# Kernel tuning notes

Measured on AMD Instinct MI355X. Metric: run time of the kernel, lower is better.

The kernel has to match this reference:

```python
import jax, jax.numpy as jnp
import numpy as np

B, N0 = 16384, 2048
NUM_CLASSES, NUM_CLUSTERS, NDIM = 12, 24, 4
W_SCALE = 0.02  # keep logits in a sane range for softmax


def setup_inputs() -> dict:
    key = jax.random.key(0)
    ks = jax.random.split(key, 7)
    return {
        "x": jax.random.normal(ks[0], (B, N0), dtype=jnp.float32),
        "W_fc": jax.random.normal(ks[1], (N0, NUM_CLASSES), dtype=jnp.float32) * W_SCALE,
        "b_fc": jax.random.normal(ks[2], (NUM_CLASSES,), dtype=jnp.float32) * W_SCALE,
        "W_bin": jax.random.normal(ks[3], (NUM_CLASSES, N0, NUM_CLUSTERS), dtype=jnp.float32) * W_SCALE,
        "b_bin": jax.random.normal(ks[4], (NUM_CLASSES, NUM_CLUSTERS), dtype=jnp.float32) * W_SCALE,
        "W_res": jax.random.normal(ks[5], (NUM_CLASSES, N0, NDIM), dtype=jnp.float32) * W_SCALE,
        "b_res": jax.random.normal(ks[6], (NUM_CLASSES, NDIM), dtype=jnp.float32) * W_SCALE,
    }


def reference(x, W_fc, b_fc, W_bin, b_bin, W_res, b_res):
    # x: [B, N0] pre-extracted features (feature_model output)
    bsz = x.shape[0]
    C = W_bin.shape[0]

    # category head
    y0 = x @ W_fc + b_fc                                   # [B, C]
    Pc = jax.nn.softmax(y0, axis=1)                        # [B, C]

    # grouped per-class bin linears as one batched GEMM -> [B, K, C]
    y1 = jnp.einsum('bd,cdk->bkc', x, W_bin) + b_bin.T[None]
    Pl = jax.nn.softmax(y1, axis=1)                        # softmax over clusters
    Plc = Pl * Pc[:, None, :]                              # [B, K, C]

    # joint argmax over (cluster, class); torch flatten of [B,K,C] -> ic = ind % C
    ind = jnp.argmax(Plc.reshape(bsz, -1), axis=1)
    ic = ind % C                                           # selected class per row

    # direct gather replaces one-hot scatter + bmm
    y1_sel = jnp.take_along_axis(y1, ic[:, None, None], axis=2)[..., 0]   # [B, K]

    # grouped per-class residual linears -> [B, ndim, C], then gather
    y2 = jnp.einsum('bd,cdn->bnc', x, W_res) + b_res.T[None]
    y2_sel = jnp.take_along_axis(y2, ic[:, None, None], axis=2)[..., 0]   # [B, ndim]

    return (y0, y1_sel, y2_sel, Plc)
```

## Files before the change

### kernel.cpp

```cpp
#include <hip/hip_runtime.h>
#include <math.h>

#define BROWS 16384
#define N0    2048
#define NCLS  12
#define NCLU  24
#define NDIM  4
#define NCOL  348
#define NPAD  384
#define NTILE 24

#define OUT0_OFF 0
#define OUT1_OFF (BROWS * NCLS)
#define OUT2_OFF (OUT1_OFF + BROWS * NCLU)
#define OUT3_OFF (OUT2_OFF + BROWS * NDIM)

typedef __attribute__((ext_vector_type(8))) short bf16x8;
typedef __attribute__((ext_vector_type(4))) float f32x4;
typedef unsigned short ushort_t;

__device__ __forceinline__ unsigned short f2bf(float f) {
    unsigned u = __float_as_uint(f);
    u += 0x7fffu + ((u >> 16) & 1u);
    return (unsigned short)(u >> 16);
}
__device__ __forceinline__ float bf2f(unsigned short h) {
    return __uint_as_float(((unsigned)h) << 16);
}
__device__ __forceinline__ void cvt8(float4 a, float4 b, bf16x8& h, bf16x8& l) {
    float f[8] = {a.x, a.y, a.z, a.w, b.x, b.y, b.z, b.w};
    #pragma unroll
    for (int i = 0; i < 8; ++i) {
        unsigned short hi = f2bf(f[i]);
        h[i] = (short)hi;
        l[i] = (short)f2bf(f[i] - bf2f(hi));
    }
}

__device__ __forceinline__ void load_lds16(const void* g, void* l) {
    __builtin_amdgcn_global_load_lds((const __attribute__((address_space(1))) void*)g,
                                     (__attribute__((address_space(3))) void*)l, 16, 0, 0);
}

__device__ __forceinline__ float fused_w(const float* __restrict__ W_fc,
                                         const float* __restrict__ W_bin,
                                         const float* __restrict__ W_res,
                                         int col, int d) {
    float w = 0.0f;
    if (col < NCLS) {
        w = W_fc[d * NCLS + col];
    } else if (col < 12 + NCLU * NCLS) {
        int jj = col - 12;
        int k = jj / NCLS, c = jj - k * NCLS;
        w = W_bin[((size_t)c * N0 + d) * NCLU + k];
    } else if (col < NCOL) {
        int jj = col - 300;
        int n = jj / NCLS, c = jj - n * NCLS;
        w = W_res[((size_t)c * N0 + d) * NDIM + n];
    }
    return w;
}

__global__ void jcp_repack3(const float* __restrict__ W_fc, const float* __restrict__ b_fc,
                            const float* __restrict__ W_bin, const float* __restrict__ b_bin,
                            const float* __restrict__ W_res, const float* __restrict__ b_res,
                            ushort_t* __restrict__ Bph, ushort_t* __restrict__ Bpl,
                            float* __restrict__ bias) {
    int t = blockIdx.x * 256 + threadIdx.x;
    if (t >= NTILE * 64 * 64) return;
    const int lane = t & 63;
    const int kb   = (t >> 6) & 63;
    const int J    = t >> 12;
    const int col  = J * 16 + (lane & 15);
    const int k0   = kb * 32 + (lane >> 4) * 8;

    bf16x8 h, l;
    #pragma unroll
    for (int i = 0; i < 8; ++i) {
        float w = fused_w(W_fc, W_bin, W_res, col, k0 + i);
        unsigned short hi = f2bf(w);
        h[i] = (short)hi;
        l[i] = (short)f2bf(w - bf2f(hi));
    }
    *(bf16x8*)(Bph + (size_t)t * 8) = h;
    *(bf16x8*)(Bpl + (size_t)t * 8) = l;

    if (t < NPAD) {
        int jb = t;
        float bv = 0.0f;
        if (jb < NCLS) {
            bv = b_fc[jb];
        } else if (jb < 12 + NCLU * NCLS) {
            int jj = jb - 12;
            int k = jj / NCLS, c = jj - k * NCLS;
            bv = b_bin[c * NCLU + k];
        } else if (jb < NCOL) {
            int jj = jb - 300;
            int n = jj / NCLS, c = jj - n * NCLS;
            bv = b_res[c * NDIM + n];
        }
        bias[jb] = bv;
    }
}

__global__ __launch_bounds__(256, 4) void jcp_gemm4(const float* __restrict__ x,
                                                    const ushort_t* __restrict__ Bph,
                                                    const ushort_t* __restrict__ Bpl,
                                                    const float* __restrict__ bias,
                                                    float* __restrict__ Y) {
    __shared__ float Lx[2 * 2048];

    const int tid  = threadIdx.x;
    const int wid  = tid >> 6;
    const int lane = tid & 63;
    const int quad = lane >> 4;
    const int l16  = lane & 15;
    const int wrow = (wid & 1) * 32;
    const int wct  = (wid >> 1) * 3;
    const int rbase = blockIdx.y * 64;
    const int jbase = blockIdx.x * 96;

    const int dr = lane >> 3;
    const int dc = (lane & 7) ^ dr;
    const float* gsrc0 = x + (size_t)(rbase + 8 * (2 * wid) + dr) * N0 + dc * 4;
    const float* gsrc1 = x + (size_t)(rbase + 8 * (2 * wid + 1) + dr) * N0 + dc * 4;
    const int ldst0 = (2 * wid) * 256;
    const int ldst1 = (2 * wid + 1) * 256;

    const int s = l16 & 7;
    const int pos1 = (2 * quad) ^ s;
    const int o1 = pos1 * 4;
    const int o2 = (pos1 ^ 1) * 4;
    const int ro0 = (wrow + l16) * 32;
    const int ro1 = (wrow + 16 + l16) * 32;

    const ushort_t* pBh = Bph + (size_t)lane * 8;
    const ushort_t* pBl = Bpl + (size_t)lane * 8;
    int Jt[3];
    #pragma unroll
    for (int j = 0; j < 3; ++j) Jt[j] = (jbase / 16 + wct + j) * 32768;

    f32x4 acc[2][3];
    #pragma unroll
    for (int i = 0; i < 2; ++i)
        #pragma unroll
        for (int j = 0; j < 3; ++j)
            acc[i][j] = f32x4{0.f, 0.f, 0.f, 0.f};

    load_lds16(gsrc0, &Lx[ldst0]);
    load_lds16(gsrc1, &Lx[ldst1]);
    __syncthreads();

    int p = 0;
    for (int it = 0; it < 64; ++it) {
        bf16x8 bh[3], bl[3];
        #pragma unroll
        for (int j = 0; j < 3; ++j) {
            bh[j] = *(const bf16x8*)(pBh + Jt[j] + it * 512);
            bl[j] = *(const bf16x8*)(pBl + Jt[j] + it * 512);
        }
        if (it < 63) {
            load_lds16(gsrc0 + (it + 1) * 32, &Lx[(p ^ 1) * 2048 + ldst0]);
            load_lds16(gsrc1 + (it + 1) * 32, &Lx[(p ^ 1) * 2048 + ldst1]);
        }
        const int pb = p * 2048;
        float4 f0a = *(const float4*)&Lx[pb + ro0 + o1];
        float4 f0b = *(const float4*)&Lx[pb + ro0 + o2];
        float4 f1a = *(const float4*)&Lx[pb + ro1 + o1];
        float4 f1b = *(const float4*)&Lx[pb + ro1 + o2];
        bf16x8 Ah[2], Al[2];
        cvt8(f0a, f0b, Ah[0], Al[0]);
        cvt8(f1a, f1b, Ah[1], Al[1]);

        #pragma unroll
        for (int j = 0; j < 3; ++j)
            #pragma unroll
            for (int i = 0; i < 2; ++i) {
                acc[i][j] = __builtin_amdgcn_mfma_f32_16x16x32_bf16(Ah[i], bh[j], acc[i][j], 0, 0, 0);
                acc[i][j] = __builtin_amdgcn_mfma_f32_16x16x32_bf16(Al[i], bh[j], acc[i][j], 0, 0, 0);
                acc[i][j] = __builtin_amdgcn_mfma_f32_16x16x32_bf16(Ah[i], bl[j], acc[i][j], 0, 0, 0);
            }
        __syncthreads();
        p ^= 1;
    }

    #pragma unroll
    for (int j = 0; j < 3; ++j) {
        const int col = jbase + wct * 16 + 16 * j + l16;
        const float bj = bias[col];
        #pragma unroll
        for (int i = 0; i < 2; ++i) {
            float* yp = Y + (size_t)(rbase + wrow + i * 16 + quad * 4) * NPAD + col;
            yp[0 * NPAD] = acc[i][j][0] + bj;
            yp[1 * NPAD] = acc[i][j][1] + bj;
            yp[2 * NPAD] = acc[i][j][2] + bj;
            yp[3 * NPAD] = acc[i][j][3] + bj;
        }
    }
}

#define LROW 388

__global__ __launch_bounds__(256) void jcp_head3(const float* __restrict__ Y,
                                                 float* __restrict__ out) {
    __shared__ float Ly[16 * LROW];
    const int tid = threadIdx.x;
    const int r0  = blockIdx.x * 16;

    #pragma unroll
    for (int jj = 0; jj < 6; ++jj) {
        int f = tid + jj * 256;
        int row = f / 96, c4 = f - row * 96;
        float4 v = *(const float4*)(Y + (size_t)(r0 + row) * NPAD + c4 * 4);
        *(float4*)&Ly[row * LROW + c4 * 4] = v;
    }
    __syncthreads();

    const int grp = tid >> 4;
    const int c   = tid & 15;
    const bool on = (c < NCLS);
    const int r   = r0 + grp;
    const float* y = &Ly[grp * LROW];

    float y0c = on ? y[c] : -INFINITY;
    float m0 = y0c;
    #pragma unroll
    for (int m = 8; m >= 1; m >>= 1) m0 = fmaxf(m0, __shfl_xor(m0, m, 16));
    float e0 = on ? expf(y0c - m0) : 0.0f;
    float s0 = e0;
    #pragma unroll
    for (int m = 8; m >= 1; m >>= 1) s0 += __shfl_xor(s0, m, 16);
    const float Pc = e0 / s0;

    float v[NCLU];
    float mc = -INFINITY;
    #pragma unroll
    for (int k = 0; k < NCLU; ++k) {
        v[k] = y[12 + k * NCLS + c];
        mc = fmaxf(mc, v[k]);
    }
    float sc = 0.0f;
    #pragma unroll
    for (int k = 0; k < NCLU; ++k) sc += expf(v[k] - mc);
    const float rs = Pc / sc;

    float y2c[NDIM];
    #pragma unroll
    for (int n = 0; n < NDIM; ++n) y2c[n] = y[300 + n * NCLS + c];

    float best = -INFINITY;
    int bk = 0;
    float* lrow = &Ly[grp * LROW];
    #pragma unroll
    for (int k = 0; k < NCLU; ++k) {
        const float p = expf(v[k] - mc) * rs;
        if (on) lrow[k * NCLS + c] = p;
        if (p > best) { best = p; bk = k; }
    }
    int flat = bk * NCLS + c;
    if (!on) { best = -INFINITY; flat = 1 << 30; }

    #pragma unroll
    for (int m = 8; m >= 1; m >>= 1) {
        const float op = __shfl_xor(best, m, 16);
        const int   of = __shfl_xor(flat, m, 16);
        if (op > best || (op == best && of < flat)) { best = op; flat = of; }
    }
    const int ic = flat % NCLS;

    if (on) out[OUT0_OFF + (size_t)r * NCLS + c] = y0c;
    if (c == ic) {
        float* o1 = out + OUT1_OFF + (size_t)r * NCLU;
        #pragma unroll
        for (int k = 0; k < NCLU; ++k) o1[k] = v[k];
        float* o2 = out + OUT2_OFF + (size_t)r * NDIM;
        #pragma unroll
        for (int n = 0; n < NDIM; ++n) o2[n] = y2c[n];
    }

    __syncthreads();
    #pragma unroll
    for (int jj = 0; jj < 5; ++jj) {
        int f = tid + jj * 256;
        if (f < 1152) {
            int row = f / 72, c4 = f - row * 72;
            *(float4*)(out + OUT3_OFF + (size_t)(r0 + row) * (NCLU * NCLS) + c4 * 4) =
                *(float4*)&Ly[row * LROW + c4 * 4];
        }
    }
}

extern "C" void kernel_launch(void* const* d_in, const int* in_sizes, int n_in,
                              void* d_out, int out_size, void* d_ws, size_t ws_size,
                              hipStream_t stream) {
    const float* x     = (const float*)d_in[0];
    const float* W_fc  = (const float*)d_in[1];
    const float* b_fc  = (const float*)d_in[2];
    const float* W_bin = (const float*)d_in[3];
    const float* b_bin = (const float*)d_in[4];
    const float* W_res = (const float*)d_in[5];
    const float* b_res = (const float*)d_in[6];
    float* out = (float*)d_out;

    ushort_t* Bph  = (ushort_t*)d_ws;
    ushort_t* Bpl  = Bph + NTILE * 64 * 64 * 8;
    float*    bias = (float*)(Bpl + NTILE * 64 * 64 * 8);
    float*    Yb   = bias + NPAD;

    jcp_repack3<<<384, 256, 0, stream>>>(W_fc, b_fc, W_bin, b_bin, W_res, b_res,
                                         Bph, Bpl, bias);
    dim3 grid(NPAD / 96, BROWS / 64);
    jcp_gemm4<<<grid, 256, 0, stream>>>(x, Bph, Bpl, bias, Yb);
    jcp_head3<<<BROWS / 16, 256, 0, stream>>>(Yb, out);
}
```

Before: 317.9 us.

## Pre-convert x to split bf16 layout and use direct LDS-loading GEMM

Adds a pass that converts x once into a swizzled hi/lo bf16 layout in workspace. A new GEMM kernel then streams that layout into LDS with async loads and runs bf16 MFMA without per-tile conversion. This removes repeated fp32 to bf16 conversion across column tiles. In exchange it adds a full extra read and write of x through memory and needs a large workspace, with a fallback to the old kernel if the workspace is too small.

```diff
diff --git a/kernel.cpp b/kernel.cpp
--- a/kernel.cpp
+++ b/kernel.cpp
@@ -103,6 +103,114 @@
     }
 }
 
+__global__ __launch_bounds__(256) void jcp_cvtx(const float* __restrict__ x,
+                                                ushort_t* __restrict__ Xp) {
+    const int t = blockIdx.x * 256 + threadIdx.x;
+    const int rec = t >> 2;
+    const int c   = t & 3;
+    const float* src = x + (size_t)rec * 32 + c * 8;
+    float4 a = *(const float4*)(src);
+    float4 b = *(const float4*)(src + 4);
+    bf16x8 h, l;
+    cvt8(a, b, h, l);
+    ushort_t* dst = Xp + (size_t)rec * 64;
+    *(bf16x8*)(dst + c * 8) = h;
+    *(bf16x8*)(dst + 32 + c * 8) = l;
+}
+
+__global__ __launch_bounds__(256, 4) void jcp_gemm5(const ushort_t* __restrict__ Xp,
+                                                    const ushort_t* __restrict__ Bph,
+                                                    const ushort_t* __restrict__ Bpl,
+                                                    const float* __restrict__ bias,
+                                                    float* __restrict__ Y) {
+    __shared__ __attribute__((aligned(16))) ushort_t Lx[2][4096];
+
+    const int tid  = threadIdx.x;
+    const int wid  = tid >> 6;
+    const int lane = tid & 63;
+    const int quad = lane >> 4;
+    const int l16  = lane & 15;
+    const int wrow = (wid & 1) * 32;
+    const int wct  = (wid >> 1) * 3;
+    const int rbase = blockIdx.y * 64;
+    const int jbase = blockIdx.x * 96;
+
+    const int r8   = lane >> 3;
+    const int cpos = lane & 7;
+    const int cs   = cpos ^ r8;
+    const ushort_t* g0 = Xp + ((size_t)(rbase + wid * 16 + r8) * 64) * 64 + cs * 8;
+    const ushort_t* g1 = Xp + ((size_t)(rbase + wid * 16 + 8 + r8) * 64) * 64 + cs * 8;
+    const int d0 = (wid * 16) * 64;
+    const int d1 = (wid * 16 + 8) * 64;
+
+    const int rm = l16 & 7;
+    const int sh = quad ^ rm;
+    const int sl = (4 + quad) ^ rm;
+    const int ro0 = (wrow + l16) * 64;
+    const int ro1 = (wrow + 16 + l16) * 64;
+
+    const ushort_t* pBh = Bph + (size_t)lane * 8;
+    const ushort_t* pBl = Bpl + (size_t)lane * 8;
+    int Jt[3];
+    #pragma unroll
+    for (int j = 0; j < 3; ++j) Jt[j] = (jbase / 16 + wct + j) * 32768;
+
+    f32x4 acc[2][3];
+    #pragma unroll
+    for (int i = 0; i < 2; ++i)
+        #pragma unroll
+        for (int j = 0; j < 3; ++j)
+            acc[i][j] = f32x4{0.f, 0.f, 0.f, 0.f};
+
+    load_lds16(g0, &Lx[0][d0]);
+    load_lds16(g1, &Lx[0][d1]);
+    __syncthreads();
+
+    int p = 0;
+    for (int it = 0; it < 64; ++it) {
+        if (it < 63) {
+            load_lds16(g0 + (it + 1) * 64, &Lx[p ^ 1][d0]);
+            load_lds16(g1 + (it + 1) * 64, &Lx[p ^ 1][d1]);
+        }
+        bf16x8 bh[3], bl[3];
+        #pragma unroll
+        for (int j = 0; j < 3; ++j) {
+            bh[j] = *(const bf16x8*)(pBh + Jt[j] + it * 512);
+            bl[j] = *(const bf16x8*)(pBl + Jt[j] + it * 512);
+        }
+        bf16x8 Ah[2], Al[2];
+        Ah[0] = *(const bf16x8*)&Lx[p][ro0 + sh * 8];
+        Al[0] = *(const bf16x8*)&Lx[p][ro0 + sl * 8];
+        Ah[1] = *(const bf16x8*)&Lx[p][ro1 + sh * 8];
+        Al[1] = *(const bf16x8*)&Lx[p][ro1 + sl * 8];
+
+        #pragma unroll
+        for (int j = 0; j < 3; ++j)
+            #pragma unroll
+            for (int i = 0; i < 2; ++i) {
+                acc[i][j] = __builtin_amdgcn_mfma_f32_16x16x32_bf16(Ah[i], bh[j], acc[i][j], 0, 0, 0);
+                acc[i][j] = __builtin_amdgcn_mfma_f32_16x16x32_bf16(Al[i], bh[j], acc[i][j], 0, 0, 0);
+                acc[i][j] = __builtin_amdgcn_mfma_f32_16x16x32_bf16(Ah[i], bl[j], acc[i][j], 0, 0, 0);
+            }
+        __syncthreads();
+        p ^= 1;
+    }
+
+    #pragma unroll
+    for (int j = 0; j < 3; ++j) {
+        const int col = jbase + wct * 16 + 16 * j + l16;
+        const float bj = bias[col];
+        #pragma unroll
+        for (int i = 0; i < 2; ++i) {
+            float* yp = Y + (size_t)(rbase + wrow + i * 16 + quad * 4) * NPAD + col;
+            yp[0 * NPAD] = acc[i][j][0] + bj;
+            yp[1 * NPAD] = acc[i][j][1] + bj;
+            yp[2 * NPAD] = acc[i][j][2] + bj;
+            yp[3 * NPAD] = acc[i][j][3] + bj;
+        }
+    }
+}
+
 __global__ __launch_bounds__(256, 4) void jcp_gemm4(const float* __restrict__ x,
                                                     const ushort_t* __restrict__ Bph,
                                                     const ushort_t* __restrict__ Bpl,
@@ -302,14 +410,22 @@
     const float* b_res = (const float*)d_in[6];
     float* out = (float*)d_out;
 
+    const size_t BP = (size_t)NTILE * 64 * 64 * 8;
     ushort_t* Bph  = (ushort_t*)d_ws;
-    ushort_t* Bpl  = Bph + NTILE * 64 * 64 * 8;
-    float*    bias = (float*)(Bpl + NTILE * 64 * 64 * 8);
+    ushort_t* Bpl  = Bph + BP;
+    float*    bias = (float*)(Bpl + BP);
     float*    Yb   = bias + NPAD;
+    ushort_t* Xp   = (ushort_t*)(Yb + (size_t)BROWS * NPAD);
+    const size_t need = (size_t)((char*)(Xp + (size_t)BROWS * 64 * 64) - (char*)d_ws);
 
     jcp_repack3<<<384, 256, 0, stream>>>(W_fc, b_fc, W_bin, b_bin, W_res, b_res,
                                          Bph, Bpl, bias);
     dim3 grid(NPAD / 96, BROWS / 64);
-    jcp_gemm4<<<grid, 256, 0, stream>>>(x, Bph, Bpl, bias, Yb);
+    if (ws_size >= need) {
+        jcp_cvtx<<<BROWS * 64 * 4 / 256, 256, 0, stream>>>(x, Xp);
+        jcp_gemm5<<<grid, 256, 0, stream>>>(Xp, Bph, Bpl, bias, Yb);
+    } else {
+        jcp_gemm4<<<grid, 256, 0, stream>>>(x, Bph, Bpl, bias, Yb);
+    }
     jcp_head3<<<BROWS / 16, 256, 0, stream>>>(Yb, out);
 }
```

After: 370.6 us. 1.17x slower.
